# Kernel optimization log

Measured on AMD Instinct MI355X. Metric: run time of the kernel, lower is better.

The kernel has to match this reference:

```python
import jax, jax.numpy as jnp
import numpy as np

B, N, D = 4, 1024, 1024
H, DH = 16, 64
N_LAYERS = 3  # len(mlp_dims) - 1 with implicit_mlp_hiddens=(64, 64)
EPS = 1.1920929e-07  # torch.nn.RMSNorm default eps = finfo(float32).eps


def _rope_tables(n, dtype):
    # lucidrains RotaryEmbedding: theta=10000, interleaved freq repeat
    inv_freq = 1.0 / (10000.0 ** (np.arange(0, DH, 2, dtype=np.float64) / DH))
    t = np.arange(n, dtype=np.float64)[:, None] * inv_freq[None, :]  # [n, DH/2]
    t = np.repeat(t, 2, axis=-1)  # [n, DH], freqs interleaved (f0,f0,f1,f1,...)
    return jnp.asarray(np.cos(t), dtype), jnp.asarray(np.sin(t), dtype)


def _rope_rotate(x, cos, sin):
    # x: [b,h,n,d]; rotate_half on interleaved pairs: (x1,x2) -> (-x2,x1)
    xp = x.reshape(*x.shape[:-1], DH // 2, 2)
    xr = jnp.stack((-xp[..., 1], xp[..., 0]), axis=-1).reshape(x.shape)
    return x * cos + xr * sin


def _attend(q, k, v):
    # rotate_queries_with_cached_keys with no cache: same positions for q and k
    n = q.shape[-2]
    cos, sin = _rope_tables(n, q.dtype)
    q = _rope_rotate(q, cos, sin)
    k = _rope_rotate(k, cos, sin)
    scale = DH ** -0.5
    scores = jnp.einsum('bhqd,bhkd->bhqk', q, k) * scale
    causal = jnp.tril(jnp.ones((n, n), dtype=bool))
    scores = jnp.where(causal, scores, -jnp.inf)
    attn = jax.nn.softmax(scores, axis=-1)
    return jnp.einsum('bhqk,bhkd->bhqd', attn, v)


def _split_heads(x):
    b, n, _ = x.shape
    return x.reshape(b, n, H, DH).transpose(0, 2, 1, 3)  # b h n d


def setup_inputs() -> dict:
    key = jax.random.key(0)
    ks = jax.random.split(key, 6)
    s = 0.02
    return {
        'tokens': jax.random.normal(ks[0], (B, N, D), jnp.float32),
        'gamma': jnp.ones((D,), jnp.float32),                                  # RMSNorm weight
        'Wq': jax.random.normal(ks[1], (D, H * DH), jnp.float32) * s,           # to_queries
        'Wk': jax.random.normal(ks[2], (N_LAYERS, D, H * DH), jnp.float32) * s, # stacked key projections
        'Wv': jax.random.normal(ks[3], (N_LAYERS, D, H * DH), jnp.float32) * s, # stacked value projections
        'Wo': jax.random.normal(ks[4], (H * DH, D), jnp.float32) * s,           # to_out
    }


def reference(tokens, gamma, Wq, Wk, Wv, Wo):
    b, n, d = tokens.shape
    # RMSNorm (prenorm)
    x = tokens * jax.lax.rsqrt(jnp.mean(tokens * tokens, axis=-1, keepdims=True) + EPS) * gamma
    out = _split_heads(x @ Wq)  # queries, [b h n d]
    for i in range(N_LAYERS):
        k = _split_heads(x @ Wk[i])
        v = _split_heads(x @ Wv[i])
        out = _attend(out, k, v)
        if i < N_LAYERS - 1:
            out = jax.nn.silu(out)  # implicit MLP activation between attention stages
    out = out.transpose(0, 2, 1, 3).reshape(b, n, H * DH)  # merge heads
    return out @ Wo
```

## Files before the change

### kernel.cpp

```cpp
#include <hip/hip_runtime.h>


typedef unsigned short u16;
typedef short s16x8 __attribute__((ext_vector_type(8)));
typedef u16 u16x4 __attribute__((ext_vector_type(4)));
typedef float f32x4 __attribute__((ext_vector_type(4)));

typedef __attribute__((address_space(1))) const unsigned int as1c_uint;
typedef __attribute__((address_space(3))) unsigned int as3_uint;

__device__ __forceinline__ float b2f(u16 h) {
  union { unsigned int u; float f; } v; v.u = ((unsigned int)h) << 16; return v.f;
}
__device__ __forceinline__ u16 f2b(float f) {
  union { float f; unsigned int u; } v; v.f = f;
  return (u16)((v.u + 0x7FFFu + ((v.u >> 16) & 1u)) >> 16);
}
__device__ __forceinline__ void gload16(const u16* g, const u16* lds) {
  __builtin_amdgcn_global_load_lds((as1c_uint*)(size_t)g,
                                   (as3_uint*)(unsigned int)(size_t)lds, 16, 0, 0);
}

__global__ __launch_bounds__(256)
void prep_kernel(const float* __restrict__ T, const float* __restrict__ gamma,
                 u16* __restrict__ X, float* __restrict__ ct,
                 float* __restrict__ st, const float* __restrict__ Wq,
                 const float* __restrict__ Wk, const float* __restrict__ Wv,
                 const float* __restrict__ Wo, u16* __restrict__ wt) {
  __shared__ float shbuf[64 * 65];
  const int bid = blockIdx.x, tid = threadIdx.x;
  if (bid < 4096) {
    const int row = bid;
    const float4 v = ((const float4*)(T + (size_t)row * 1024))[tid];
    float ss = v.x * v.x + v.y * v.y + v.z * v.z + v.w * v.w;
#pragma unroll
    for (int msk = 1; msk <= 32; msk <<= 1) ss += __shfl_xor(ss, msk, 64);
    if ((tid & 63) == 0) shbuf[tid >> 6] = ss;
    __syncthreads();
    const float tot = shbuf[0] + shbuf[1] + shbuf[2] + shbuf[3];
    const float r = rsqrtf(tot * (1.0f / 1024.0f) + 1.1920929e-07f);
    const float4 gm = ((const float4*)gamma)[tid];
    u16x4 o;
    o[0] = f2b(v.x * r * gm.x); o[1] = f2b(v.y * r * gm.y);
    o[2] = f2b(v.z * r * gm.z); o[3] = f2b(v.w * r * gm.w);
    *(u16x4*)(X + (size_t)row * 1024 + tid * 4) = o;
  } else if (bid < 4224) {
    const int idx = (bid - 4096) * 256 + tid;
    const int n = idx >> 5, j = idx & 31;
    const double freq = pow(10000.0, -(double)j / 32.0);
    const double a = (double)n * freq;
    ct[idx] = (float)cos(a);
    st[idx] = (float)sin(a);
  } else {
    const int t = bid - 4224;
    const int z = t >> 8, rem = t & 255;
    const float* src = (z == 0) ? Wq
                     : (z <= 3) ? (Wk + (size_t)(z - 1) * 1048576)
                     : (z <= 6) ? (Wv + (size_t)(z - 4) * 1048576)
                                : Wo;
    u16* dst = wt + (size_t)z * 1048576;
    const int bx = (rem & 15) * 64;
    const int by = (rem >> 4) * 64;
    const int tcol = (tid & 15) * 4, trow = tid >> 4;
#pragma unroll
    for (int i = 0; i < 4; ++i) {
      const int r = trow + i * 16;
      const float4 v = *(const float4*)(src + (size_t)(bx + r) * 1024 + by + tcol);
      shbuf[r * 65 + tcol] = v.x; shbuf[r * 65 + tcol + 1] = v.y;
      shbuf[r * 65 + tcol + 2] = v.z; shbuf[r * 65 + tcol + 3] = v.w;
    }
    __syncthreads();
    const int k4 = (tid & 15) * 4;
#pragma unroll
    for (int j2 = 0; j2 < 4; ++j2) {
      const int R = (tid >> 4) + j2 * 16;
      u16x4 o;
      o[0] = f2b(shbuf[k4 * 65 + R]);       o[1] = f2b(shbuf[(k4 + 1) * 65 + R]);
      o[2] = f2b(shbuf[(k4 + 2) * 65 + R]); o[3] = f2b(shbuf[(k4 + 3) * 65 + R]);
      *(u16x4*)&dst[(size_t)(by + R) * 1024 + bx + k4] = o;
    }
  }
}

template <int KIND>
__global__ __launch_bounds__(256, 2)
void gemm_kernel(const u16* __restrict__ A, const u16* __restrict__ Bt,
                 void* __restrict__ Cout, const float* __restrict__ ct,
                 const float* __restrict__ st) {
  constexpr int MB = (KIND == 0) ? 8 : 4;
  constexpr int NB = (KIND == 0) ? 4 : 2;
  constexpr int BM = MB * 32;
  constexpr int BN = NB * 32;
  constexpr int ASLOT = BM * 32;
  constexpr int SLOT = (BM + BN) * 32;
  const int p = blockIdx.x;
  const int role = (p & 7) * (KIND == 0 ? 112 : 64) + (p >> 3);
  int z, m0, n0;
  if (KIND == 0) {
    z = role >> 7;
    const int rem = role & 127;
    m0 = (rem >> 3) * BM;
    n0 = (rem & 7) * BN;
  } else {
    z = 0;
    m0 = (role >> 4) * BM;
    n0 = (role & 15) * BN;
  }

  const int tid = threadIdx.x;
  const int w = tid >> 6, l = tid & 63;
  const int g = l >> 4, ll = l & 15;
  const int wr = w >> 1, wc = w & 1;

  const u16* Ab = A + (size_t)m0 * 1024;
  const u16* Bb = Bt + (size_t)z * 1048576 + (size_t)n0 * 1024;

  __shared__ u16 SH[3][SLOT];

  const f32x4 zero = {0.f, 0.f, 0.f, 0.f};
  f32x4 acc[MB][NB];
#pragma unroll
  for (int i = 0; i < MB; ++i)
#pragma unroll
    for (int j = 0; j < NB; ++j) acc[i][j] = zero;

  auto stage = [&](int t2) {
    const int slot = t2 % 3;
    const int k0 = t2 * 32;
    const int rsub = l >> 2, sl = l & 3;
#pragma unroll
    for (int c = 0; c < MB / 2; ++c) {
      const int chunk = c * 4 + w;
      const int row = chunk * 16 + rsub;
      const int kk = k0 + ((sl ^ ((row >> 1) & 3)) << 3);
      gload16(Ab + (size_t)row * 1024 + kk, &SH[slot][chunk * 512]);
    }
#pragma unroll
    for (int c = 0; c < BN / 64; ++c) {
      const int chunk = c * 4 + w;
      const int row = chunk * 16 + rsub;
      const int kk = k0 + ((sl ^ ((row >> 1) & 3)) << 3);
      gload16(Bb + (size_t)row * 1024 + kk, &SH[slot][ASLOT + chunk * 512]);
    }
  };

  const int NT = 32;
  stage(0); stage(1);

#pragma unroll
  for (int t = 0; t < NT; ++t) {
    if (t < NT - 1) {
      if constexpr (KIND == 0) asm volatile("s_waitcnt vmcnt(6)" ::: "memory");
      else                     asm volatile("s_waitcnt vmcnt(3)" ::: "memory");
    } else {
      asm volatile("s_waitcnt vmcnt(0)" ::: "memory");
    }
    __builtin_amdgcn_s_barrier();

    const int slot = t % 3;
    const u16* As = &SH[slot][0];
    const u16* Bs = &SH[slot][ASLOT];
    s16x8 bfr[NB];
#pragma unroll
    for (int nf = 0; nf < NB; ++nf) {
      const int row = wc * (NB * 16) + nf * 16 + ll;
      bfr[nf] = *(const s16x8*)&Bs[row * 32 + ((g ^ ((row >> 1) & 3)) << 3)];
    }
    s16x8 af[MB];
#pragma unroll
    for (int mf = 0; mf < MB; ++mf) {
      const int row = wr * (MB * 16) + mf * 16 + ll;
      af[mf] = *(const s16x8*)&As[row * 32 + ((g ^ ((row >> 1) & 3)) << 3)];
    }

    if (t + 2 < NT) stage(t + 2);

    __builtin_amdgcn_s_setprio(1);
#pragma unroll
    for (int mf = 0; mf < MB; ++mf)
#pragma unroll
      for (int nf = 0; nf < NB; ++nf)
        acc[mf][nf] = __builtin_amdgcn_mfma_f32_16x16x32_bf16(af[mf], bfr[nf],
                                                              acc[mf][nf], 0, 0, 0);
    __builtin_amdgcn_s_setprio(0);
  }
  __syncthreads();

  if (KIND == 0) {
    u16* C = (u16*)Cout + (size_t)z * 4194304;
    if (z < 4) {
      const bool doRope = (z >= 1);
      u16* T = &SH[0][0];
#pragma unroll
      for (int mf = 0; mf < MB; ++mf)
#pragma unroll
        for (int nf = 0; nf < NB; ++nf) {
          const int c = wc * 64 + nf * 16 + ll;
#pragma unroll
          for (int rg = 0; rg < 4; ++rg) {
            const int r = wr * (MB * 16) + mf * 16 + g * 4 + rg;
            T[r * 128 + (c ^ ((r & 7) << 4))] = f2b(acc[mf][nf][rg]);
          }
        }
      __syncthreads();
#pragma unroll
      for (int i = 0; i < BM / 16; ++i) {
        const int R = (tid >> 4) + i * 16;
        const int c0 = (tid & 15) * 8;
        s16x8 v = *(const s16x8*)&T[R * 128 + (c0 ^ ((R & 7) << 4))];
        if (doRope) {
          const int n = (m0 + R) & 1023;
          const int j0 = (c0 & 63) >> 1;
          const float4 c4 = *(const float4*)(ct + n * 32 + j0);
          const float4 s4 = *(const float4*)(st + n * 32 + j0);
          s16x8 vo;
#pragma unroll
          for (int pp = 0; pp < 4; ++pp) {
            const float c = ((const float*)&c4)[pp];
            const float s = ((const float*)&s4)[pp];
            const float x0 = b2f((u16)v[2 * pp]), x1 = b2f((u16)v[2 * pp + 1]);
            vo[2 * pp]     = (short)f2b(x0 * c - x1 * s);
            vo[2 * pp + 1] = (short)f2b(x1 * c + x0 * s);
          }
          v = vo;
        }
        *(s16x8*)&C[(size_t)(m0 + R) * 1024 + n0 + c0] = v;
      }
    } else {
#pragma unroll
      for (int mf = 0; mf < MB; ++mf)
#pragma unroll
        for (int nf = 0; nf < NB; ++nf) {
          const int col = n0 + wc * 64 + nf * 16 + ll;
          const int hh = col >> 6, d = col & 63;
          const int mb = m0 + wr * (MB * 16) + mf * 16 + g * 4;
          const int bb = mb >> 10, n = mb & 1023;
          u16x4 pk;
#pragma unroll
          for (int rg = 0; rg < 4; ++rg) pk[rg] = f2b(acc[mf][nf][rg]);
          *(u16x4*)&C[((size_t)((bb * 16 + hh) * 64 + d)) * 1024 + n] = pk;
        }
    }
  } else {
    float* C = (float*)Cout;
#pragma unroll
    for (int mf = 0; mf < MB; ++mf)
#pragma unroll
      for (int nf = 0; nf < NB; ++nf) {
        const int col = n0 + wc * (NB * 16) + nf * 16 + ll;
#pragma unroll
        for (int rg = 0; rg < 4; ++rg) {
          const int m = m0 + wr * (MB * 16) + mf * 16 + g * 4 + rg;
          C[(size_t)m * 1024 + col] = acc[mf][nf][rg];
        }
      }
  }
}

template <int SILU>
__global__ __launch_bounds__(256)
void attn_kernel(const u16* __restrict__ Q, const u16* __restrict__ K,
                 const u16* __restrict__ Vt, u16* __restrict__ O,
                 const float* __restrict__ ct, const float* __restrict__ st) {
  const int lin = blockIdx.x + (blockIdx.y << 3);
  const int role = (lin & 7) * 64 + (lin >> 3);
  const int p = role & 7, bh = role >> 3;
  const int q_lo = p, q_hi = 15 - p;
  const int b = bh >> 4, h = bh & 15;
  const int tid = threadIdx.x, w = tid >> 6, l = tid & 63;
  const int g = l >> 4, ll = l & 15;

  const u16* Qb = Q + (size_t)(b * 1024) * 1024 + h * 64;
  const u16* Kb = K + (size_t)(b * 1024) * 1024 + h * 64;
  const u16* Vb = Vt + (size_t)((b * 16 + h) * 64) * 1024;
  u16* Ob = O + (size_t)(b * 1024) * 1024 + h * 64;

  __shared__ u16 Ksh[2][128 * 72];
  __shared__ u16 Psh[4][16 * 72];

  s16x8 qfL[2], qfH[2];
  auto loadQ = [&](int qt, s16x8* qf) {
    const int qrow = qt * 64 + w * 16 + ll;
#pragma unroll
    for (int kc = 0; kc < 2; ++kc) {
      const int d0 = kc * 32 + g * 8;
      const int j0 = d0 >> 1;
      const float4 c4 = *(const float4*)(ct + qrow * 32 + j0);
      const float4 s4v = *(const float4*)(st + qrow * 32 + j0);
      const s16x8 qin = *(const s16x8*)(Qb + (size_t)qrow * 1024 + d0);
      s16x8 qo;
#pragma unroll
      for (int pp = 0; pp < 4; ++pp) {
        const float c = ((const float*)&c4)[pp], s = ((const float*)&s4v)[pp];
        const float x0 = b2f((u16)qin[2 * pp]), x1 = b2f((u16)qin[2 * pp + 1]);
        qo[2 * pp]     = (short)f2b((x0 * c - x1 * s) * 0.125f);
        qo[2 * pp + 1] = (short)f2b((x1 * c + x0 * s) * 0.125f);
      }
      qf[kc] = qo;
    }
  };
  loadQ(q_lo, qfL);
  loadQ(q_hi, qfH);

  float lsL[4], lsH[4];
  f32x4 oL[4], oH[4];
  const f32x4 zero = {0.f, 0.f, 0.f, 0.f};
#pragma unroll
  for (int rg = 0; rg < 4; ++rg) { lsL[rg] = 0.f; lsH[rg] = 0.f; }
#pragma unroll
  for (int df = 0; df < 4; ++df) { oL[df] = zero; oH[df] = zero; }

  const int srow = tid >> 2;
  const int sc0 = (tid & 3) * 16;

  s16x8 kr0, kr1, kr2, kr3;
  auto kload = [&](int tt) {
    const u16* kp = Kb + (size_t)(tt * 128 + srow) * 1024 + sc0;
    kr0 = *(const s16x8*)kp;
    kr1 = *(const s16x8*)(kp + 8);
    const u16* kp2 = kp + (size_t)64 * 1024;
    kr2 = *(const s16x8*)kp2;
    kr3 = *(const s16x8*)(kp2 + 8);
  };
  auto kstore = [&](int bf) {
    *(s16x8*)&Ksh[bf][srow * 72 + sc0] = kr0;
    *(s16x8*)&Ksh[bf][srow * 72 + sc0 + 8] = kr1;
    *(s16x8*)&Ksh[bf][(64 + srow) * 72 + sc0] = kr2;
    *(s16x8*)&Ksh[bf][(64 + srow) * 72 + sc0 + 8] = kr3;
  };

  kload(0);
  kstore(0);
  __syncthreads();
  int buf = 0;

  const int iters = (q_hi + 2) >> 1;
  for (int tt = 0; tt < iters; ++tt) {
    const bool pre = (tt + 1 < iters);
    if (pre) kload(tt + 1);

    s16x8 vb[2][2][4];
#pragma unroll
    for (int sub = 0; sub < 2; ++sub)
#pragma unroll
      for (int kc = 0; kc < 2; ++kc)
#pragma unroll
        for (int df = 0; df < 4; ++df)
          vb[sub][kc][df] = *(const s16x8*)(Vb + (size_t)(df * 16 + ll) * 1024 +
                                           (tt * 2 + sub) * 64 + kc * 32 + g * 8);

    auto process = [&](const s16x8* qf, float* ls, f32x4* o, int sub,
                       bool diag) {
      const int rb = sub * 64;
      f32x4 s4[4];
#pragma unroll
      for (int nf = 0; nf < 4; ++nf) {
        const s16x8 kb0 = *(const s16x8*)&Ksh[buf][(rb + nf * 16 + ll) * 72 + g * 8];
        const s16x8 kb1 = *(const s16x8*)&Ksh[buf][(rb + nf * 16 + ll) * 72 + 32 + g * 8];
        f32x4 sv = zero;
        sv = __builtin_amdgcn_mfma_f32_16x16x32_bf16(qf[0], kb0, sv, 0, 0, 0);
        sv = __builtin_amdgcn_mfma_f32_16x16x32_bf16(qf[1], kb1, sv, 0, 0, 0);
        s4[nf] = sv;
      }

      if (diag) {
#pragma unroll
        for (int nf = 0; nf < 4; ++nf)
#pragma unroll
          for (int rg = 0; rg < 4; ++rg)
            if (nf * 16 + ll > w * 16 + g * 4 + rg) s4[nf][rg] = -3.0e38f;
      }

#pragma unroll
      for (int rg = 0; rg < 4; ++rg) {
        float ps = 0.f;
#pragma unroll
        for (int nf = 0; nf < 4; ++nf) {
          const float pv = __expf(s4[nf][rg] - 12.f);
          s4[nf][rg] = pv;
          ps += pv;
        }
        ls[rg] += ps;
      }

#pragma unroll
      for (int nf = 0; nf < 4; ++nf)
#pragma unroll
        for (int rg = 0; rg < 4; ++rg)
          Psh[w][(g * 4 + rg) * 72 + nf * 16 + ll] = f2b(s4[nf][rg]);

#pragma unroll
      for (int kc = 0; kc < 2; ++kc) {
        const s16x8 pa = *(const s16x8*)&Psh[w][ll * 72 + kc * 32 + g * 8];
#pragma unroll
        for (int df = 0; df < 4; ++df)
          o[df] = __builtin_amdgcn_mfma_f32_16x16x32_bf16(pa, vb[sub][kc][df],
                                                          o[df], 0, 0, 0);
      }
    };

    const int ka = 2 * tt, kb2 = 2 * tt + 1;
    process(qfH, lsH, oH, 0, ka == q_hi);
    if (kb2 <= q_hi) process(qfH, lsH, oH, 1, kb2 == q_hi);
    if (ka <= q_lo) process(qfL, lsL, oL, 0, ka == q_lo);
    if (kb2 <= q_lo) process(qfL, lsL, oL, 1, kb2 == q_lo);

    if (pre) kstore(buf ^ 1);
    __syncthreads();
    buf ^= 1;
  }

  auto finish = [&](float* ls, f32x4* o, int qt) {
#pragma unroll
    for (int rg = 0; rg < 4; ++rg) {
      float v = ls[rg];
      v += __shfl_xor(v, 1, 64);
      v += __shfl_xor(v, 2, 64);
      v += __shfl_xor(v, 4, 64);
      v += __shfl_xor(v, 8, 64);
      ls[rg] = 1.f / v;
    }
#pragma unroll
    for (int df = 0; df < 4; ++df)
#pragma unroll
      for (int rg = 0; rg < 4; ++rg) {
        float val = o[df][rg] * ls[rg];
        if (SILU) val = val / (1.f + __expf(-val));
        Ob[(size_t)(qt * 64 + w * 16 + g * 4 + rg) * 1024 + df * 16 + ll] =
            f2b(val);
      }
  };
  finish(lsH, oH, q_hi);
  finish(lsL, oL, q_lo);
}

extern "C" void kernel_launch(void* const* d_in, const int* in_sizes, int n_in,
                              void* d_out, int out_size, void* d_ws, size_t ws_size,
                              hipStream_t stream) {
  (void)in_sizes; (void)n_in; (void)out_size; (void)ws_size;
  const float* tokens = (const float*)d_in[0];
  const float* gamma  = (const float*)d_in[1];
  const float* Wq     = (const float*)d_in[2];
  const float* Wk     = (const float*)d_in[3];
  const float* Wv     = (const float*)d_in[4];
  const float* Wo     = (const float*)d_in[5];
  float* out = (float*)d_out;

  u16* x    = (u16*)d_ws;
  u16* wt   = x + (size_t)4096 * 1024;
  u16* qkv  = wt + (size_t)8 * 1048576;
  u16* outA = qkv + (size_t)7 * 4194304;
  u16* outB = outA + 4194304;
  float* ct = (float*)(outB + 4194304);
  float* st = ct + 32768;

  prep_kernel<<<6272, 256, 0, stream>>>(tokens, gamma, x, ct, st,
                                        Wq, Wk, Wv, Wo, wt);
  gemm_kernel<0><<<896, 256, 0, stream>>>(x, wt, qkv, ct, st);

  const size_t M4 = 4194304;
  attn_kernel<1><<<dim3(8, 64), 256, 0, stream>>>(qkv, qkv + 1 * M4, qkv + 4 * M4,
                                                  outA, ct, st);
  attn_kernel<1><<<dim3(8, 64), 256, 0, stream>>>(outA, qkv + 2 * M4, qkv + 5 * M4,
                                                  outB, ct, st);
  attn_kernel<0><<<dim3(8, 64), 256, 0, stream>>>(outB, qkv + 3 * M4, qkv + 6 * M4,
                                                  outA, ct, st);

  gemm_kernel<1><<<512, 256, 0, stream>>>(outA, wt + (size_t)7 * 1048576,
                                          (void*)out, ct, st);
}
```

Measured before the change: 218.3 us.

## Compute transposed scores so P stays in registers, dropping the LDS round-trip

The attention kernel now computes S^T (K as the A operand, Q as B), so each lane holds probabilities for a single query row. Those probabilities are packed to bf16 with v_cvt_pk_bf16_f32 and fed directly as the B operand of the PV MFMA, with V as A. This removes the per-warp Psh shared-memory write/read and its layout shuffle, and replaces per-row sums with one scalar per lane. V loads now happen per sub-tile, split into two 8-byte halves to match the k-permuted register layout. Output stores become 8-byte packed writes along d, at the cost of smaller, less coalesced V loads.

```diff
diff --git a/kernel.cpp b/kernel.cpp
--- a/kernel.cpp
+++ b/kernel.cpp
@@ -3,6 +3,7 @@
 
 typedef unsigned short u16;
 typedef short s16x8 __attribute__((ext_vector_type(8)));
+typedef short s16x4 __attribute__((ext_vector_type(4)));
 typedef u16 u16x4 __attribute__((ext_vector_type(4)));
 typedef float f32x4 __attribute__((ext_vector_type(4)));
 
@@ -15,6 +16,11 @@
 __device__ __forceinline__ u16 f2b(float f) {
   union { float f; unsigned int u; } v; v.f = f;
   return (u16)((v.u + 0x7FFFu + ((v.u >> 16) & 1u)) >> 16);
+}
+__device__ __forceinline__ unsigned cvtpk(float lo, float hi) {
+  unsigned r;
+  asm("v_cvt_pk_bf16_f32 %0, %1, %2" : "=v"(r) : "v"(lo), "v"(hi));
+  return r;
 }
 __device__ __forceinline__ void gload16(const u16* g, const u16* lds) {
   __builtin_amdgcn_global_load_lds((as1c_uint*)(size_t)g,
@@ -276,7 +282,6 @@
   u16* Ob = O + (size_t)(b * 1024) * 1024 + h * 64;
 
   __shared__ u16 Ksh[2][128 * 72];
-  __shared__ u16 Psh[4][16 * 72];
 
   s16x8 qfL[2], qfH[2];
   auto loadQ = [&](int qt, s16x8* qf) {
@@ -302,11 +307,9 @@
   loadQ(q_lo, qfL);
   loadQ(q_hi, qfH);
 
-  float lsL[4], lsH[4];
+  float lsL = 0.f, lsH = 0.f;
   f32x4 oL[4], oH[4];
   const f32x4 zero = {0.f, 0.f, 0.f, 0.f};
-#pragma unroll
-  for (int rg = 0; rg < 4; ++rg) { lsL[rg] = 0.f; lsH[rg] = 0.f; }
 #pragma unroll
   for (int df = 0; df < 4; ++df) { oL[df] = zero; oH[df] = zero; }
 
@@ -339,96 +342,102 @@
     const bool pre = (tt + 1 < iters);
     if (pre) kload(tt + 1);
 
-    s16x8 vb[2][2][4];
-#pragma unroll
-    for (int sub = 0; sub < 2; ++sub)
-#pragma unroll
-      for (int kc = 0; kc < 2; ++kc)
+#pragma unroll
+    for (int sub = 0; sub < 2; ++sub) {
+      const int ks = 2 * tt + sub;
+      if (ks > q_hi) break;
+      const int rb = sub * 64;
+      const int t64 = ks * 64;
+
+      s16x8 va[2][4];
+#pragma unroll
+      for (int c = 0; c < 2; ++c)
+#pragma unroll
+        for (int df = 0; df < 4; ++df) {
+          union { s16x4 h[2]; s16x8 v; } tv;
+          const u16* vp = Vb + (size_t)(df * 16 + ll) * 1024 + t64 + c * 32 + g * 4;
+          tv.h[0] = *(const s16x4*)vp;
+          tv.h[1] = *(const s16x4*)(vp + 16);
+          va[c][df] = tv.v;
+        }
+
+      auto process = [&](const s16x8* qf, float* ls, f32x4* o, bool diag) {
+        f32x4 s4[4];
+#pragma unroll
+        for (int nf = 0; nf < 4; ++nf) {
+          const s16x8 kb0 = *(const s16x8*)&Ksh[buf][(rb + nf * 16 + ll) * 72 + g * 8];
+          const s16x8 kb1 = *(const s16x8*)&Ksh[buf][(rb + nf * 16 + ll) * 72 + 32 + g * 8];
+          f32x4 sv = zero;
+          sv = __builtin_amdgcn_mfma_f32_16x16x32_bf16(kb0, qf[0], sv, 0, 0, 0);
+          sv = __builtin_amdgcn_mfma_f32_16x16x32_bf16(kb1, qf[1], sv, 0, 0, 0);
+          s4[nf] = sv;
+        }
+
+        if (diag) {
+#pragma unroll
+          for (int nf = 0; nf < 4; ++nf)
+#pragma unroll
+            for (int rg = 0; rg < 4; ++rg)
+              if (nf * 16 + g * 4 + rg > w * 16 + ll) s4[nf][rg] = -3.0e38f;
+        }
+
+        float ps = 0.f;
+#pragma unroll
+        for (int nf = 0; nf < 4; ++nf)
+#pragma unroll
+          for (int rg = 0; rg < 4; ++rg) {
+            const float pv = __expf(s4[nf][rg] - 12.f);
+            s4[nf][rg] = pv;
+            ps += pv;
+          }
+        *ls += ps;
+
+        union { unsigned u[4]; s16x8 v; } pk0, pk1;
+        pk0.u[0] = cvtpk(s4[0][0], s4[0][1]);
+        pk0.u[1] = cvtpk(s4[0][2], s4[0][3]);
+        pk0.u[2] = cvtpk(s4[1][0], s4[1][1]);
+        pk0.u[3] = cvtpk(s4[1][2], s4[1][3]);
+        pk1.u[0] = cvtpk(s4[2][0], s4[2][1]);
+        pk1.u[1] = cvtpk(s4[2][2], s4[2][3]);
+        pk1.u[2] = cvtpk(s4[3][0], s4[3][1]);
+        pk1.u[3] = cvtpk(s4[3][2], s4[3][3]);
+
 #pragma unroll
         for (int df = 0; df < 4; ++df)
-          vb[sub][kc][df] = *(const s16x8*)(Vb + (size_t)(df * 16 + ll) * 1024 +
-                                           (tt * 2 + sub) * 64 + kc * 32 + g * 8);
-
-    auto process = [&](const s16x8* qf, float* ls, f32x4* o, int sub,
-                       bool diag) {
-      const int rb = sub * 64;
-      f32x4 s4[4];
-#pragma unroll
-      for (int nf = 0; nf < 4; ++nf) {
-        const s16x8 kb0 = *(const s16x8*)&Ksh[buf][(rb + nf * 16 + ll) * 72 + g * 8];
-        const s16x8 kb1 = *(const s16x8*)&Ksh[buf][(rb + nf * 16 + ll) * 72 + 32 + g * 8];
-        f32x4 sv = zero;
-        sv = __builtin_amdgcn_mfma_f32_16x16x32_bf16(qf[0], kb0, sv, 0, 0, 0);
-        sv = __builtin_amdgcn_mfma_f32_16x16x32_bf16(qf[1], kb1, sv, 0, 0, 0);
-        s4[nf] = sv;
-      }
-
-      if (diag) {
-#pragma unroll
-        for (int nf = 0; nf < 4; ++nf)
-#pragma unroll
-          for (int rg = 0; rg < 4; ++rg)
-            if (nf * 16 + ll > w * 16 + g * 4 + rg) s4[nf][rg] = -3.0e38f;
-      }
-
-#pragma unroll
-      for (int rg = 0; rg < 4; ++rg) {
-        float ps = 0.f;
-#pragma unroll
-        for (int nf = 0; nf < 4; ++nf) {
-          const float pv = __expf(s4[nf][rg] - 12.f);
-          s4[nf][rg] = pv;
-          ps += pv;
-        }
-        ls[rg] += ps;
-      }
-
-#pragma unroll
-      for (int nf = 0; nf < 4; ++nf)
-#pragma unroll
-        for (int rg = 0; rg < 4; ++rg)
-          Psh[w][(g * 4 + rg) * 72 + nf * 16 + ll] = f2b(s4[nf][rg]);
-
-#pragma unroll
-      for (int kc = 0; kc < 2; ++kc) {
-        const s16x8 pa = *(const s16x8*)&Psh[w][ll * 72 + kc * 32 + g * 8];
+          o[df] = __builtin_amdgcn_mfma_f32_16x16x32_bf16(va[0][df], pk0.v,
+                                                          o[df], 0, 0, 0);
 #pragma unroll
         for (int df = 0; df < 4; ++df)
-          o[df] = __builtin_amdgcn_mfma_f32_16x16x32_bf16(pa, vb[sub][kc][df],
+          o[df] = __builtin_amdgcn_mfma_f32_16x16x32_bf16(va[1][df], pk1.v,
                                                           o[df], 0, 0, 0);
-      }
-    };
-
-    const int ka = 2 * tt, kb2 = 2 * tt + 1;
-    process(qfH, lsH, oH, 0, ka == q_hi);
-    if (kb2 <= q_hi) process(qfH, lsH, oH, 1, kb2 == q_hi);
-    if (ka <= q_lo) process(qfL, lsL, oL, 0, ka == q_lo);
-    if (kb2 <= q_lo) process(qfL, lsL, oL, 1, kb2 == q_lo);
+      };
+
+      process(qfH, &lsH, oH, ks == q_hi);
+      if (ks <= q_lo) process(qfL, &lsL, oL, ks == q_lo);
+    }
 
     if (pre) kstore(buf ^ 1);
     __syncthreads();
     buf ^= 1;
   }
 
-  auto finish = [&](float* ls, f32x4* o, int qt) {
-#pragma unroll
-    for (int rg = 0; rg < 4; ++rg) {
-      float v = ls[rg];
-      v += __shfl_xor(v, 1, 64);
-      v += __shfl_xor(v, 2, 64);
-      v += __shfl_xor(v, 4, 64);
-      v += __shfl_xor(v, 8, 64);
-      ls[rg] = 1.f / v;
-    }
-#pragma unroll
-    for (int df = 0; df < 4; ++df)
+  auto finish = [&](float ls, f32x4* o, int qt) {
+    float v = ls;
+    v += __shfl_xor(v, 16, 64);
+    v += __shfl_xor(v, 32, 64);
+    const float inv = 1.f / v;
+    const size_t rowoff = (size_t)(qt * 64 + w * 16 + ll) * 1024;
+#pragma unroll
+    for (int df = 0; df < 4; ++df) {
+      u16x4 pk;
 #pragma unroll
       for (int rg = 0; rg < 4; ++rg) {
-        float val = o[df][rg] * ls[rg];
+        float val = o[df][rg] * inv;
         if (SILU) val = val / (1.f + __expf(-val));
-        Ob[(size_t)(qt * 64 + w * 16 + g * 4 + rg) * 1024 + df * 16 + ll] =
-            f2b(val);
+        pk[rg] = f2b(val);
       }
+      *(u16x4*)&Ob[rowoff + df * 16 + g * 4] = pk;
+    }
   };
   finish(lsH, oH, q_hi);
   finish(lsL, oL, q_lo);
```

Measured after the change: 298.6 us. +36.8%, slower.
